# Performance work log

Measured on AMD Instinct MI355X. Metric: run time of the kernel, lower is better.

Reference implementation:

```python
import jax, jax.numpy as jnp
import numpy as np

B, S, E = 2048, 23, 768
RED, H, NUM_LABELS = 256, 8, 25
DH = RED // H
DELTA = 0.1
EPS_LN = 1e-5


def setup_inputs() -> dict:
    key = jax.random.key(0)
    ks = jax.random.split(key, 20)
    g = lambda k, shape, fan: jax.random.normal(k, shape, dtype=jnp.float32) * (1.0 / np.sqrt(fan))
    inp = {
        'cls_embeddings': jax.random.normal(ks[0], (B, S, E), dtype=jnp.float32),
        'existing_mask': jax.random.randint(ks[1], (B, S), 0, 2, dtype=jnp.int32),
        'missing_emb': g(ks[2], (S, E), E),
        'W1': g(ks[3], (E // 2, E), E), 'b1': jnp.zeros((E // 2,), jnp.float32),
        'W2': g(ks[4], (RED, E // 2), E // 2), 'b2': jnp.zeros((RED,), jnp.float32),
        'ln_g': jnp.ones((RED,), jnp.float32), 'ln_b': jnp.zeros((RED,), jnp.float32),
        'Wq': g(ks[5], (RED, RED), RED), 'bq': jnp.zeros((RED,), jnp.float32),
        'Wk': g(ks[6], (RED, RED), RED), 'bk': jnp.zeros((RED,), jnp.float32),
        'Wv': g(ks[7], (RED, RED), RED), 'bv': jnp.zeros((RED,), jnp.float32),
        'Wo': g(ks[8], (RED, RED), RED), 'bo': jnp.zeros((RED,), jnp.float32),
        'Wp': g(ks[9], (NUM_LABELS, RED), RED), 'bp': jnp.zeros((NUM_LABELS,), jnp.float32),
    }
    return inp


def _layer_norm(x, g, b):
    mu = jnp.mean(x, axis=-1, keepdims=True)
    var = jnp.mean(jnp.square(x - mu), axis=-1, keepdims=True)
    return (x - mu) * jax.lax.rsqrt(var + EPS_LN) * g + b


def _forward(cls_embeddings, existing_mask, missing_emb, W1, b1, W2, b2, ln_g, ln_b,
             Wq, bq, Wk, bk, Wv, bv, Wo, bo, Wp, bp):
    exist = existing_mask > 0                              # [B,S] bool
    # Gather: existing sections use BERT CLS, missing slots use learned embeddings
    sec = jnp.where(exist[..., None], cls_embeddings, missing_emb[None])  # [B,S,E]
    # SectionDimReducer (exact-erf GELU as in nn.GELU default)
    h = jax.nn.gelu(sec @ W1.T + b1, approximate=False)
    h = jax.nn.gelu(h @ W2.T + b2, approximate=False)
    red = _layer_norm(h, ln_g, ln_b)                       # [B,S,RED]
    # Tiny MHA: every slot queries the existing sections of its own EHR
    q = (red @ Wq.T + bq).reshape(B, S, H, DH)
    k = (red @ Wk.T + bk).reshape(B, S, H, DH)
    v = (red @ Wv.T + bv).reshape(B, S, H, DH)
    scores = jnp.einsum('bqhd,bkhd->bhqk', q, k) / np.sqrt(DH)
    scores = jnp.where(exist[:, None, None, :], scores, -1e9)
    attn = jax.nn.softmax(scores, axis=-1)                 # [B,H,S,S]
    ctx = jnp.einsum('bhqk,bkhd->bqhd', attn, v).reshape(B, S, RED)
    mha_out = ctx @ Wo.T + bo                              # [B,S,RED]
    # Scatter: only missing slots (of EHRs with >=1 existing section) are replaced
    any_exist = jnp.any(exist, axis=1)                     # [B]
    use_attn = (~exist) & any_exist[:, None]               # [B,S]
    updated = jnp.where(use_attn[..., None], mha_out, red)
    # margin-based orthogonality loss on section embeddings
    norm = updated / jnp.maximum(jnp.linalg.norm(updated, axis=-1, keepdims=True), 1e-8)
    gram = jnp.einsum('bid,bjd->bij', norm, norm)          # [B,S,S]
    off = 1.0 - jnp.eye(S, dtype=updated.dtype)
    loss_orth = jnp.sum(jax.nn.relu(jnp.abs(gram) - DELTA) * off) / (B * S * (S - 1))
    logits = updated.mean(axis=1) @ Wp.T + bp              # [B,NUM_LABELS]
    return loss_orth, logits


def reference(cls_embeddings, existing_mask, missing_emb, W1, b1, W2, b2, ln_g, ln_b,
              Wq, bq, Wk, bk, Wv, bv, Wo, bo, Wp, bp):
    return _forward(cls_embeddings, existing_mask, missing_emb, W1, b1, W2, b2, ln_g, ln_b,
                    Wq, bq, Wk, bk, Wv, bv, Wo, bo, Wp, bp)
```

## Files before the change

kernel.cpp:

```cpp
#include <hip/hip_runtime.h>

typedef unsigned short u16;
typedef unsigned int u32;
typedef __attribute__((ext_vector_type(8))) short short8;
typedef __attribute__((ext_vector_type(4))) float f32x4;

struct __align__(8) us4 { u16 x, y, z, w; };

__device__ __forceinline__ float bf1(u16 v){ return __uint_as_float(((u32)v) << 16); }
__device__ __forceinline__ float bflo(u32 u){ return __uint_as_float(u << 16); }
__device__ __forceinline__ float bfhi(u32 u){ return __uint_as_float(u & 0xFFFF0000u); }
__device__ __forceinline__ u16 fbf(float f){
    u32 u = __float_as_uint(f);
    return (u16)((u + 0x7FFFu + ((u >> 16) & 1u)) >> 16);
}
__device__ __forceinline__ float gelu_exact(float x){
    return 0.5f * x * (1.0f + erff(x * 0.70710678118654752f));
}
__device__ __forceinline__ void unp8(uint4 u, float* f){
    f[0]=bflo(u.x); f[1]=bfhi(u.x); f[2]=bflo(u.y); f[3]=bfhi(u.y);
    f[4]=bflo(u.z); f[5]=bfhi(u.z); f[6]=bflo(u.w); f[7]=bfhi(u.w);
}
__device__ __forceinline__ uint4 pack8(float4 a, float4 b){
    uint4 u;
    u.x = (u32)fbf(a.x) | ((u32)fbf(a.y) << 16);
    u.y = (u32)fbf(a.z) | ((u32)fbf(a.w) << 16);
    u.z = (u32)fbf(b.x) | ((u32)fbf(b.y) << 16);
    u.w = (u32)fbf(b.z) | ((u32)fbf(b.w) << 16);
    return u;
}

#define MFMA16(a, b, c) __builtin_amdgcn_mfma_f32_16x16x32_bf16(a, b, c, 0, 0, 0)
#define QSTR 264
#define CAPROWS 46208


__global__ __launch_bounds__(256) void wconv(
    const float* __restrict__ W1, const float* __restrict__ W2,
    const float* __restrict__ Wq, const float* __restrict__ Wk,
    const float* __restrict__ Wv, const float* __restrict__ Wo,
    const float* __restrict__ Wp, u16* __restrict__ dst,
    const int* __restrict__ mask, int* __restrict__ idx,
    int* __restrict__ rowsrc, int* __restrict__ cnt)
{
    const int i = blockIdx.x * 256 + threadIdx.x;
    if (i < 47104) {
        if (i < 23) rowsrc[i] = -(i + 1);
        if (mask[i] > 0) {
            const int slot = 23 + atomicAdd(cnt, 1);
            idx[i] = slot;
            rowsrc[slot] = i;
        }
    }
    const float* s; int o;
    if      (i < 294912) { s = W1; o = i; }
    else if (i < 393216) { s = W2; o = i - 294912; }
    else if (i < 458752) { s = Wq; o = i - 393216; }
    else if (i < 524288) { s = Wk; o = i - 458752; }
    else if (i < 589824) { s = Wv; o = i - 524288; }
    else if (i < 655360) { s = Wo; o = i - 589824; }
    else                 { s = Wp; o = i - 655360; }
    dst[i] = fbf(s[o]);
}

__global__ __launch_bounds__(256) void gemm1_kernel(
    const float* __restrict__ cls, const int* __restrict__ rowsrc,
    const int* __restrict__ cnt, const float* __restrict__ missing,
    const u16* __restrict__ W, const float* __restrict__ bias,
    u16* __restrict__ C)
{
    const int K = 768, M = 384;
    const int nBase = blockIdx.y * 128;
    if (nBase >= *cnt + 23) return;
    __shared__ u16 As[128 * 40];
    __shared__ u16 Bs[128 * 40];
    const int tid = threadIdx.x;
    const int w = tid >> 6, lane = tid & 63;
    const int mBase = blockIdx.x * 128;
    const int wr = w >> 1, wc = w & 1;
    const int r0 = tid >> 2;
    const int co = (tid & 3) * 8;
    const int frow = lane & 15, quad = lane >> 4;

    const int rs0 = rowsrc[nBase + r0];
    const int rs1 = rowsrc[nBase + r0 + 64];
    const float* ap0 = (rs0 >= 0) ? cls + (size_t)rs0 * 768
                                  : missing + (size_t)(-rs0 - 1) * 768;
    const float* ap1 = (rs1 >= 0) ? cls + (size_t)rs1 * 768
                                  : missing + (size_t)(-rs1 - 1) * 768;
    const u16* bp0 = W + (size_t)(mBase + r0) * K;
    const u16* bp1 = W + (size_t)(mBase + r0 + 64) * K;

    f32x4 acc[4][4];
#pragma unroll
    for (int mt = 0; mt < 4; ++mt)
#pragma unroll
        for (int nt = 0; nt < 4; ++nt) acc[mt][nt] = f32x4{0.f, 0.f, 0.f, 0.f};

    float4 a0a = *(const float4*)(ap0 + co), a0b = *(const float4*)(ap0 + co + 4);
    float4 a1a = *(const float4*)(ap1 + co), a1b = *(const float4*)(ap1 + co + 4);
    uint4 pb0 = *(const uint4*)(bp0 + co), pb1 = *(const uint4*)(bp1 + co);

    for (int k0 = 0; k0 < K; k0 += 32) {
        __syncthreads();
        *(uint4*)(As + r0 * 40 + co) = pack8(a0a, a0b);
        *(uint4*)(As + (r0 + 64) * 40 + co) = pack8(a1a, a1b);
        *(uint4*)(Bs + r0 * 40 + co) = pb0;
        *(uint4*)(Bs + (r0 + 64) * 40 + co) = pb1;
        __syncthreads();
        if (k0 + 32 < K) {
            const int kn = k0 + 32 + co;
            a0a = *(const float4*)(ap0 + kn); a0b = *(const float4*)(ap0 + kn + 4);
            a1a = *(const float4*)(ap1 + kn); a1b = *(const float4*)(ap1 + kn + 4);
            pb0 = *(const uint4*)(bp0 + kn);  pb1 = *(const uint4*)(bp1 + kn);
        }
        short8 af[4], bfv[4];
#pragma unroll
        for (int mt = 0; mt < 4; ++mt)
            af[mt] = *(const short8*)(As + (wr * 64 + mt * 16 + frow) * 40 + quad * 8);
#pragma unroll
        for (int nt = 0; nt < 4; ++nt)
            bfv[nt] = *(const short8*)(Bs + (wc * 64 + nt * 16 + frow) * 40 + quad * 8);
#pragma unroll
        for (int mt = 0; mt < 4; ++mt)
#pragma unroll
            for (int nt = 0; nt < 4; ++nt)
                acc[mt][nt] = MFMA16(af[mt], bfv[nt], acc[mt][nt]);
    }

#pragma unroll
    for (int nt = 0; nt < 4; ++nt) {
        const int col = mBase + wc * 64 + nt * 16 + frow;
        const float bv = bias[col];
#pragma unroll
        for (int mt = 0; mt < 4; ++mt)
#pragma unroll
            for (int reg = 0; reg < 4; ++reg) {
                const int row = nBase + wr * 64 + mt * 16 + quad * 4 + reg;
                C[(size_t)row * M + col] = fbf(gelu_exact(acc[mt][nt][reg] + bv));
            }
    }
}

__global__ __launch_bounds__(256) void gemm_bt(
    const u16* __restrict__ A, const u16* __restrict__ W,
    const float* __restrict__ bias, u16* __restrict__ C, int K, int M,
    const int* __restrict__ cnt)
{
    const int nBase = blockIdx.y * 128;
    if (nBase >= *cnt + 23) return;
    __shared__ u16 As[128 * 40];
    __shared__ u16 Bs[128 * 40];
    const int tid = threadIdx.x;
    const int w = tid >> 6, lane = tid & 63;
    const int mBase = blockIdx.x * 128;
    const int wr = w >> 1, wc = w & 1;
    const int r0 = tid >> 2;
    const int co = (tid & 3) * 8;
    const int frow = lane & 15, quad = lane >> 4;

    f32x4 acc[4][4];
#pragma unroll
    for (int mt = 0; mt < 4; ++mt)
#pragma unroll
        for (int nt = 0; nt < 4; ++nt) acc[mt][nt] = f32x4{0.f, 0.f, 0.f, 0.f};

    uint4 pa0 = *(const uint4*)(A + (size_t)(nBase + r0) * K + co);
    uint4 pa1 = *(const uint4*)(A + (size_t)(nBase + r0 + 64) * K + co);
    uint4 pb0 = *(const uint4*)(W + (size_t)(mBase + r0) * K + co);
    uint4 pb1 = *(const uint4*)(W + (size_t)(mBase + r0 + 64) * K + co);

    for (int k0 = 0; k0 < K; k0 += 32) {
        __syncthreads();
        *(uint4*)(As + r0 * 40 + co) = pa0;
        *(uint4*)(As + (r0 + 64) * 40 + co) = pa1;
        *(uint4*)(Bs + r0 * 40 + co) = pb0;
        *(uint4*)(Bs + (r0 + 64) * 40 + co) = pb1;
        __syncthreads();
        if (k0 + 32 < K) {
            const int kn = k0 + 32 + co;
            pa0 = *(const uint4*)(A + (size_t)(nBase + r0) * K + kn);
            pa1 = *(const uint4*)(A + (size_t)(nBase + r0 + 64) * K + kn);
            pb0 = *(const uint4*)(W + (size_t)(mBase + r0) * K + kn);
            pb1 = *(const uint4*)(W + (size_t)(mBase + r0 + 64) * K + kn);
        }
        short8 af[4], bfv[4];
#pragma unroll
        for (int mt = 0; mt < 4; ++mt)
            af[mt] = *(const short8*)(As + (wr * 64 + mt * 16 + frow) * 40 + quad * 8);
#pragma unroll
        for (int nt = 0; nt < 4; ++nt)
            bfv[nt] = *(const short8*)(Bs + (wc * 64 + nt * 16 + frow) * 40 + quad * 8);
#pragma unroll
        for (int mt = 0; mt < 4; ++mt)
#pragma unroll
            for (int nt = 0; nt < 4; ++nt)
                acc[mt][nt] = MFMA16(af[mt], bfv[nt], acc[mt][nt]);
    }

#pragma unroll
    for (int nt = 0; nt < 4; ++nt) {
        const int col = mBase + wc * 64 + nt * 16 + frow;
        const float bv = bias[col];
#pragma unroll
        for (int mt = 0; mt < 4; ++mt)
#pragma unroll
            for (int reg = 0; reg < 4; ++reg) {
                const int row = nBase + wr * 64 + mt * 16 + quad * 4 + reg;
                C[(size_t)row * M + col] = fbf(gelu_exact(acc[mt][nt][reg] + bv));
            }
    }
}

__device__ __forceinline__ void ln1_reg(
    const float* x, const float4& g0, const float4& g1,
    const float4& b0, const float4& b1, u16* rp)
{
    float s = x[0] + x[1] + x[2] + x[3] + x[4] + x[5] + x[6] + x[7];
    s += __shfl_xor(s, 1); s += __shfl_xor(s, 2); s += __shfl_xor(s, 4);
    s += __shfl_xor(s, 8); s += __shfl_xor(s, 16);
    const float mu = s * (1.f / 256.f);
    float v = 0.f;
#pragma unroll
    for (int e = 0; e < 8; ++e) { const float d = x[e] - mu; v += d * d; }
    v += __shfl_xor(v, 1); v += __shfl_xor(v, 2); v += __shfl_xor(v, 4);
    v += __shfl_xor(v, 8); v += __shfl_xor(v, 16);
    const float rs = rsqrtf(v * (1.f / 256.f) + 1e-5f);
    float4 ya, yb;
    ya.x = (x[0]-mu)*rs*g0.x + b0.x;
    ya.y = (x[1]-mu)*rs*g0.y + b0.y;
    ya.z = (x[2]-mu)*rs*g0.z + b0.z;
    ya.w = (x[3]-mu)*rs*g0.w + b0.w;
    yb.x = (x[4]-mu)*rs*g1.x + b1.x;
    yb.y = (x[5]-mu)*rs*g1.y + b1.y;
    yb.z = (x[6]-mu)*rs*g1.z + b1.z;
    yb.w = (x[7]-mu)*rs*g1.w + b1.w;
    *(uint4*)rp = pack8(ya, yb);
}

__device__ __forceinline__ void ln3_reg_store(
    uint4 rg0, uint4 rg1, uint4 rg2, bool has2,
    const float* __restrict__ lng, const float* __restrict__ lnb,
    u16* dstBase, int s0, int c0o)
{
    const float4 g0 = *(const float4*)(lng + c0o);
    const float4 g1 = *(const float4*)(lng + c0o + 4);
    const float4 b0 = *(const float4*)(lnb + c0o);
    const float4 b1 = *(const float4*)(lnb + c0o + 4);
    float x[8];
    unp8(rg0, x); ln1_reg(x, g0, g1, b0, b1, dstBase + s0 * QSTR + c0o);
    unp8(rg1, x); ln1_reg(x, g0, g1, b0, b1, dstBase + (s0 + 8) * QSTR + c0o);
    if (has2) { unp8(rg2, x); ln1_reg(x, g0, g1, b0, b1, dstBase + (s0 + 16) * QSTR + c0o); }
}

#define KLOOP_PF(WPTR, SRC, ACC)                                                  \
    {                                                                             \
        short8 nb0 = *(const short8*)(WPTR);                                      \
        short8 nb1 = *(const short8*)((WPTR) + 16 * 256);                         \
        short8 nb2 = *(const short8*)((WPTR) + 32 * 256);                         \
        short8 nb3 = *(const short8*)((WPTR) + 48 * 256);                         \
        for (int k0 = 0; k0 < 256; k0 += 32) {                                    \
            short8 a0 = *(const short8*)((SRC) + r0c * QSTR + k0 + quad * 8);     \
            short8 a1 = *(const short8*)((SRC) + r1c * QSTR + k0 + quad * 8);     \
            short8 c0 = nb0, c1 = nb1, c2 = nb2, c3 = nb3;                        \
            if (k0 + 32 < 256) {                                                  \
                nb0 = *(const short8*)((WPTR) + (k0 + 32));                       \
                nb1 = *(const short8*)((WPTR) + 16 * 256 + (k0 + 32));            \
                nb2 = *(const short8*)((WPTR) + 32 * 256 + (k0 + 32));            \
                nb3 = *(const short8*)((WPTR) + 48 * 256 + (k0 + 32));            \
            }                                                                     \
            ACC[0][0] = MFMA16(a0, c0, ACC[0][0]); ACC[1][0] = MFMA16(a1, c0, ACC[1][0]); \
            ACC[0][1] = MFMA16(a0, c1, ACC[0][1]); ACC[1][1] = MFMA16(a1, c1, ACC[1][1]); \
            ACC[0][2] = MFMA16(a0, c2, ACC[0][2]); ACC[1][2] = MFMA16(a1, c2, ACC[1][2]); \
            ACC[0][3] = MFMA16(a0, c3, ACC[0][3]); ACC[1][3] = MFMA16(a1, c3, ACC[1][3]); \
        }                                                                         \
    }

__global__ __launch_bounds__(256, 3) void attn_tail_kernel(
    const u16* __restrict__ redb, const int* __restrict__ mask,
    const int* __restrict__ idxArr,
    const u16* __restrict__ Wqkvb,
    const float* __restrict__ bq, const float* __restrict__ bk,
    const float* __restrict__ bv, const u16* __restrict__ Wob,
    const float* __restrict__ bo, const float* __restrict__ lng,
    const float* __restrict__ lnb, const u16* __restrict__ Wpb,
    const float* __restrict__ bp, float* __restrict__ out,
    float* __restrict__ lossAcc)
{
    __shared__ __align__(16) unsigned char SM[40960];
    u16* s_rq = (u16*)SM;
    u16* s_k  = (u16*)(SM + 12144);
    u16* s_vT = (u16*)(SM + 24288);
    int* sEx   = (int*)(SM + 40672);
    int* sMiss = (int*)(SM + 40764);
    int* sCrow = (int*)(SM + 40856);
    float* sDiag = (float*)(SM + 24288);
    float* sInv  = (float*)(SM + 24384);
    float* sPool = (float*)(SM + 24480);

    const int b = blockIdx.x, t = threadIdx.x;
    const int w = t >> 6, lane = t & 63;
    const int frow = lane & 15, quad = lane >> 4;
    const int r0c = frow;
    const int r1c = (16 + frow > 22) ? 22 : 16 + frow;
    const f32x4 z4 = f32x4{0.f, 0.f, 0.f, 0.f};

    {
        const int myEx = (t < 23) ? mask[b * 23 + t] : 0;
        if (t < 23) {
            sEx[t] = myEx;
            sCrow[t] = (myEx > 0) ? idxArr[b * 23 + t] : t;
        }
        if (t < 64) {
            const unsigned long long ball = __ballot((t < 23) && (myEx > 0));
            if (t < 23) sMiss[t] = (ball != 0ull && myEx <= 0) ? 1 : 0;
        }
    }
    for (int i = t; i < 1024; i += 256) ((uint4*)s_vT)[i] = make_uint4(0u, 0u, 0u, 0u);
    __syncthreads();

    {
        const int s0 = t >> 5, c0o = (t & 31) * 8;
        uint4 rg0 = *(const uint4*)(redb + (size_t)sCrow[s0] * 256 + c0o);
        uint4 rg1 = *(const uint4*)(redb + (size_t)sCrow[s0 + 8] * 256 + c0o);
        uint4 rg2 = make_uint4(0u, 0u, 0u, 0u);
        const bool has2 = t < 224;
        if (has2) rg2 = *(const uint4*)(redb + (size_t)sCrow[s0 + 16] * 256 + c0o);
        ln3_reg_store(rg0, rg1, rg2, has2, lng, lnb, s_rq, s0, c0o);
    }
    __syncthreads();

    const int cmb = w * 64 + frow;
    {
        f32x4 ka[2][4];
#pragma unroll
        for (int mt = 0; mt < 2; ++mt)
#pragma unroll
            for (int nt = 0; nt < 4; ++nt) ka[mt][nt] = z4;
        const u16* wp = Wqkvb + (size_t)(256 + cmb) * 256 + quad * 8;
        const float bb[4] = {bk[cmb], bk[cmb + 16], bk[cmb + 32], bk[cmb + 48]};
        KLOOP_PF(wp, s_rq, ka)
#pragma unroll
        for (int nt = 0; nt < 4; ++nt) {
            const int cm = cmb + nt * 16;
#pragma unroll
            for (int mt = 0; mt < 2; ++mt)
#pragma unroll
                for (int reg = 0; reg < 4; ++reg) {
                    const int s = mt * 16 + quad * 4 + reg;
                    if (s < 23) s_k[s * QSTR + cm] = fbf(ka[mt][nt][reg] + bb[nt]);
                }
        }
    }
    {
        f32x4 va[2][4];
#pragma unroll
        for (int mt = 0; mt < 2; ++mt)
#pragma unroll
            for (int nt = 0; nt < 4; ++nt) va[mt][nt] = z4;
        const u16* wp = Wqkvb + (size_t)(512 + cmb) * 256 + quad * 8;
        const float bb[4] = {bv[cmb], bv[cmb + 16], bv[cmb + 32], bv[cmb + 48]};
        KLOOP_PF(wp, s_rq, va)
#pragma unroll
        for (int nt = 0; nt < 4; ++nt) {
            const int cm = cmb + nt * 16;
#pragma unroll
            for (int mt = 0; mt < 2; ++mt)
#pragma unroll
                for (int reg = 0; reg < 4; ++reg) {
                    const int s = mt * 16 + quad * 4 + reg;
                    if (s < 23) s_vT[cm * 32 + s] = fbf(va[mt][nt][reg] + bb[nt]);
                }
        }
    }
    {
        f32x4 qa[2][4];
#pragma unroll
        for (int mt = 0; mt < 2; ++mt)
#pragma unroll
            for (int nt = 0; nt < 4; ++nt) qa[mt][nt] = z4;
        const u16* wp = Wqkvb + (size_t)cmb * 256 + quad * 8;
        const float bb[4] = {bq[cmb], bq[cmb + 16], bq[cmb + 32], bq[cmb + 48]};
        KLOOP_PF(wp, s_rq, qa)
        __syncthreads();
#pragma unroll
        for (int nt = 0; nt < 4; ++nt) {
            const int cm = cmb + nt * 16;
#pragma unroll
            for (int mt = 0; mt < 2; ++mt)
#pragma unroll
                for (int reg = 0; reg < 4; ++reg) {
                    const int s = mt * 16 + quad * 4 + reg;
                    if (s < 23) s_rq[s * QSTR + cm] = fbf(qa[mt][nt][reg] + bb[nt]);
                }
        }
    }

    {
        const float scl = 0.17677669529663687f;
        const float m0 = (sEx[frow] > 0) ? 0.f : -1e9f;
        const float m1 = (16 + frow < 23 && sEx[16 + frow] > 0) ? 0.f : -1e9f;
#pragma unroll
        for (int hh2 = 0; hh2 < 2; ++hh2) {
            const int hb = w * 64 + hh2 * 32;
            short8 aq0 = *(const short8*)(s_rq + r0c * QSTR + hb + quad * 8);
            short8 aq1 = *(const short8*)(s_rq + r1c * QSTR + hb + quad * 8);
            short8 bk0 = *(const short8*)(s_k + r0c * QSTR + hb + quad * 8);
            short8 bk1 = *(const short8*)(s_k + r1c * QSTR + hb + quad * 8);
            f32x4 s00 = MFMA16(aq0, bk0, z4);
            f32x4 s01 = MFMA16(aq0, bk1, z4);
            f32x4 s10 = MFMA16(aq1, bk0, z4);
            f32x4 s11 = MFMA16(aq1, bk1, z4);
#pragma unroll
            for (int mt = 0; mt < 2; ++mt) {
                f32x4& c0 = mt ? s10 : s00;
                f32x4& c1 = mt ? s11 : s01;
#pragma unroll
                for (int reg = 0; reg < 4; ++reg) {
                    float v0 = c0[reg] * scl + m0;
                    float v1 = c1[reg] * scl + m1;
                    float mx = fmaxf(v0, v1);
#pragma unroll
                    for (int m = 8; m; m >>= 1) mx = fmaxf(mx, __shfl_xor(mx, m));
                    float p0 = __expf(v0 - mx), p1 = __expf(v1 - mx);
                    float sm = p0 + p1;
#pragma unroll
                    for (int m = 8; m; m >>= 1) sm += __shfl_xor(sm, m);
                    const float inv = 1.f / sm;
                    c0[reg] = p0 * inv;
                    c1[reg] = p1 * inv;
                }
            }
#pragma unroll
            for (int reg = 0; reg < 4; ++reg) {
                const int q0r = quad * 4 + reg;
                s_k[q0r * QSTR + hb + frow]      = fbf(s00[reg]);
                s_k[q0r * QSTR + hb + 16 + frow] = fbf(s01[reg]);
                const int q1r = 16 + quad * 4 + reg;
                if (q1r < 23) {
                    s_k[q1r * QSTR + hb + frow]      = fbf(s10[reg]);
                    s_k[q1r * QSTR + hb + 16 + frow] = fbf(s11[reg]);
                }
            }
            short8 pa0 = *(const short8*)(s_k + r0c * QSTR + hb + quad * 8);
            short8 pa1 = *(const short8*)(s_k + r1c * QSTR + hb + quad * 8);
            short8 bv0 = *(const short8*)(s_vT + (hb + frow) * 32 + quad * 8);
            short8 bv1 = *(const short8*)(s_vT + (hb + 16 + frow) * 32 + quad * 8);
            f32x4 c00 = MFMA16(pa0, bv0, z4);
            f32x4 c01 = MFMA16(pa0, bv1, z4);
            f32x4 c10 = MFMA16(pa1, bv0, z4);
            f32x4 c11 = MFMA16(pa1, bv1, z4);
#pragma unroll
            for (int reg = 0; reg < 4; ++reg) {
                const int q0r = quad * 4 + reg;
                s_rq[q0r * QSTR + hb + frow]      = fbf(c00[reg]);
                s_rq[q0r * QSTR + hb + 16 + frow] = fbf(c01[reg]);
                const int q1r = 16 + quad * 4 + reg;
                if (q1r < 23) {
                    s_rq[q1r * QSTR + hb + frow]      = fbf(c10[reg]);
                    s_rq[q1r * QSTR + hb + 16 + frow] = fbf(c11[reg]);
                }
            }
        }
    }
    __syncthreads();

    {
        f32x4 wacc[2][4];
#pragma unroll
        for (int mt = 0; mt < 2; ++mt)
#pragma unroll
            for (int nt = 0; nt < 4; ++nt) wacc[mt][nt] = z4;
        const u16* wp = Wob + (size_t)cmb * 256 + quad * 8;
        const float ob[4] = {bo[cmb], bo[cmb + 16], bo[cmb + 32], bo[cmb + 48]};
        KLOOP_PF(wp, s_rq, wacc)
        {
            const int s0 = t >> 5, c0o = (t & 31) * 8;
            uint4 rg0 = *(const uint4*)(redb + (size_t)sCrow[s0] * 256 + c0o);
            uint4 rg1 = *(const uint4*)(redb + (size_t)sCrow[s0 + 8] * 256 + c0o);
            uint4 rg2 = make_uint4(0u, 0u, 0u, 0u);
            const bool has2 = t < 224;
            if (has2) rg2 = *(const uint4*)(redb + (size_t)sCrow[s0 + 16] * 256 + c0o);
            ln3_reg_store(rg0, rg1, rg2, has2, lng, lnb, s_k, s0, c0o);
        }
        __syncthreads();
#pragma unroll
        for (int nt = 0; nt < 4; ++nt) {
            const int col = cmb + nt * 16;
#pragma unroll
            for (int mt = 0; mt < 2; ++mt)
#pragma unroll
                for (int reg = 0; reg < 4; ++reg) {
                    const int s = mt * 16 + quad * 4 + reg;
                    if (s < 23 && sMiss[s])
                        s_k[s * QSTR + col] = fbf(wacc[mt][nt][reg] + ob[nt]);
                }
        }
    }
    __syncthreads();

    f32x4 g00 = z4, g01 = z4, g10 = z4, g11 = z4;
    if (w == 0) {
        short8 ga0 = *(const short8*)(s_k + r0c * QSTR + quad * 8);
        short8 ga1 = *(const short8*)(s_k + r1c * QSTR + quad * 8);
        for (int k0 = 0; k0 < 256; k0 += 32) {
            short8 a0 = ga0, a1 = ga1;
            if (k0 + 32 < 256) {
                ga0 = *(const short8*)(s_k + r0c * QSTR + k0 + 32 + quad * 8);
                ga1 = *(const short8*)(s_k + r1c * QSTR + k0 + 32 + quad * 8);
            }
            g00 = MFMA16(a0, a0, g00);
            g01 = MFMA16(a0, a1, g01);
            g10 = MFMA16(a1, a0, g10);
            g11 = MFMA16(a1, a1, g11);
        }
#pragma unroll
        for (int reg = 0; reg < 4; ++reg) {
            if (frow == quad * 4 + reg) {
                sDiag[frow] = g00[reg];
                if (16 + frow < 23) sDiag[16 + frow] = g11[reg];
            }
        }
    } else {
        for (int c = t - 64; c < 256; c += 192) {
            float pv = 0.f;
#pragma unroll
            for (int s = 0; s < 23; ++s) pv += bf1(s_k[s * QSTR + c]);
            sPool[c] = pv * (1.f / 23.f);
        }
    }
    __syncthreads();
    if (t < 23) sInv[t] = 1.f / fmaxf(sqrtf(sDiag[t]), 1e-8f);
    __syncthreads();

    if (w == 0) {
        float contrib = 0.f;
        const float ic0 = sInv[frow];
        const float ic1 = (16 + frow < 23) ? sInv[16 + frow] : 0.f;
        const bool c1ok = (16 + frow < 23);
#pragma unroll
        for (int reg = 0; reg < 4; ++reg) {
            const int rA = quad * 4 + reg;
            const float irA = sInv[rA];
            if (rA != frow) {
                const float cc = fabsf(g00[reg] * irA * ic0) - 0.1f;
                if (cc > 0.f) contrib += cc;
            }
            if (c1ok) {
                const float cc = fabsf(g01[reg] * irA * ic1) - 0.1f;
                if (cc > 0.f) contrib += cc;
            }
            const int rB = 16 + quad * 4 + reg;
            if (rB < 23) {
                const float irB = sInv[rB];
                {
                    const float cc = fabsf(g10[reg] * irB * ic0) - 0.1f;
                    if (cc > 0.f) contrib += cc;
                }
                if (c1ok && rB != 16 + frow) {
                    const float cc = fabsf(g11[reg] * irB * ic1) - 0.1f;
                    if (cc > 0.f) contrib += cc;
                }
            }
        }
#pragma unroll
        for (int m = 32; m; m >>= 1) contrib += __shfl_xor(contrib, m);
        if (lane == 0) atomicAdd(lossAcc, contrib);
    } else {
        const int li = t - 64;
        {
            const int L = li >> 3, chunk = li & 7;
            float a = 0.f;
#pragma unroll
            for (int q4 = 0; q4 < 4; ++q4) {
                const int c8 = chunk * 4 + q4;
                float wf[8]; unp8(*(const uint4*)(Wpb + (size_t)L * 256 + c8 * 8), wf);
                const float4 p0 = *(const float4*)(sPool + c8 * 8);
                const float4 p1 = *(const float4*)(sPool + c8 * 8 + 4);
                a += wf[0] * p0.x + wf[1] * p0.y + wf[2] * p0.z + wf[3] * p0.w
                   + wf[4] * p1.x + wf[5] * p1.y + wf[6] * p1.z + wf[7] * p1.w;
            }
            a += __shfl_xor(a, 1); a += __shfl_xor(a, 2); a += __shfl_xor(a, 4);
            if (chunk == 0) out[1 + b * 25 + L] = a + bp[L];
        }
        if (li < 8) {
            float a = 0.f;
#pragma unroll
            for (int q4 = 0; q4 < 4; ++q4) {
                const int c8 = li * 4 + q4;
                float wf[8]; unp8(*(const uint4*)(Wpb + (size_t)24 * 256 + c8 * 8), wf);
                const float4 p0 = *(const float4*)(sPool + c8 * 8);
                const float4 p1 = *(const float4*)(sPool + c8 * 8 + 4);
                a += wf[0] * p0.x + wf[1] * p0.y + wf[2] * p0.z + wf[3] * p0.w
                   + wf[4] * p1.x + wf[5] * p1.y + wf[6] * p1.z + wf[7] * p1.w;
            }
            a += __shfl_xor(a, 1); a += __shfl_xor(a, 2); a += __shfl_xor(a, 4);
            if (li == 0) out[1 + b * 25 + 24] = a + bp[24];
        }
    }
}

__global__ void loss_finalize(const float* __restrict__ lossAcc, float* __restrict__ out)
{
    out[0] = lossAcc[0] * (1.f / 1036288.f);
}

extern "C" void kernel_launch(void* const* d_in, const int* in_sizes, int n_in,
                              void* d_out, int out_size, void* d_ws, size_t ws_size,
                              hipStream_t stream)
{
    const float* cls     = (const float*)d_in[0];
    const int*   mask    = (const int*)d_in[1];
    const float* missing = (const float*)d_in[2];
    const float* W1 = (const float*)d_in[3];  const float* b1 = (const float*)d_in[4];
    const float* W2 = (const float*)d_in[5];  const float* b2 = (const float*)d_in[6];
    const float* lng = (const float*)d_in[7]; const float* lnb = (const float*)d_in[8];
    const float* Wq = (const float*)d_in[9];  const float* bq = (const float*)d_in[10];
    const float* Wk = (const float*)d_in[11]; const float* bk = (const float*)d_in[12];
    const float* Wv = (const float*)d_in[13]; const float* bv = (const float*)d_in[14];
    const float* Wo = (const float*)d_in[15]; const float* bo = (const float*)d_in[16];
    const float* Wp = (const float*)d_in[17]; const float* bp = (const float*)d_in[18];
    float* out = (float*)d_out;

    char* ws = (char*)d_ws;
    u16* h1b  = (u16*)ws;
    u16* redb = (u16*)(ws + 35487744);
    u16* Wb   = (u16*)(ws + 59146240);
    u16* W1b   = Wb;
    u16* W2b   = Wb + 294912;
    u16* Wqkvb = Wb + 393216;
    u16* Wob   = Wb + 589824;
    u16* Wpb   = Wb + 655360;
    int* idx    = (int*)(ws + 60469760);
    int* rowsrc = (int*)(ws + 60658176);
    int* cnt    = (int*)(ws + 60843008);
    float* lossAcc = (float*)(ws + 60843012);

    hipMemsetAsync(cnt, 0, 8, stream);
    hipMemsetAsync(rowsrc, 0, CAPROWS * sizeof(int), stream);

    wconv<<<2585, 256, 0, stream>>>(W1, W2, Wq, Wk, Wv, Wo, Wp, Wb,
                                    mask, idx, rowsrc, cnt);
    gemm1_kernel<<<dim3(3, 361), 256, 0, stream>>>(cls, rowsrc, cnt, missing,
                                                   W1b, b1, h1b);
    gemm_bt<<<dim3(2, 361), 256, 0, stream>>>(h1b, W2b, b2, redb, 384, 256, cnt);
    attn_tail_kernel<<<2048, 256, 0, stream>>>(redb, mask, idx, Wqkvb, bq, bk, bv,
                                               Wob, bo, lng, lnb, Wpb, bp,
                                               out, lossAcc);
    loss_finalize<<<1, 1, 0, stream>>>(lossAcc, out);
}
```

Baseline: 501.4 us.

## Double-buffer A tiles and load W fragments directly into registers in GEMMs

Both GEMM kernels now double-buffer the A tile in shared memory, so each k-step needs one barrier instead of two. The B (weight) operand no longer goes through shared memory: each lane loads its MFMA fragment straight from global memory into registers and prefetches the next step's fragment. This removes LDS traffic and a sync per iteration. In exchange it issues more global loads of the weight matrix, since the two warp rows duplicate them, and raises register pressure.

```diff
diff --git a/kernel.cpp b/kernel.cpp
--- a/kernel.cpp
+++ b/kernel.cpp
@@ -72,8 +72,7 @@
     const int K = 768, M = 384;
     const int nBase = blockIdx.y * 128;
     if (nBase >= *cnt + 23) return;
-    __shared__ u16 As[128 * 40];
-    __shared__ u16 Bs[128 * 40];
+    __shared__ u16 As[2][128 * 40];
     const int tid = threadIdx.x;
     const int w = tid >> 6, lane = tid & 63;
     const int mBase = blockIdx.x * 128;
@@ -88,8 +87,7 @@
                                   : missing + (size_t)(-rs0 - 1) * 768;
     const float* ap1 = (rs1 >= 0) ? cls + (size_t)rs1 * 768
                                   : missing + (size_t)(-rs1 - 1) * 768;
-    const u16* bp0 = W + (size_t)(mBase + r0) * K;
-    const u16* bp1 = W + (size_t)(mBase + r0 + 64) * K;
+    const u16* wpB = W + (size_t)(mBase + wc * 64 + frow) * K + quad * 8;
 
     f32x4 acc[4][4];
 #pragma unroll
@@ -97,35 +95,50 @@
 #pragma unroll
         for (int nt = 0; nt < 4; ++nt) acc[mt][nt] = f32x4{0.f, 0.f, 0.f, 0.f};
 
-    float4 a0a = *(const float4*)(ap0 + co), a0b = *(const float4*)(ap0 + co + 4);
-    float4 a1a = *(const float4*)(ap1 + co), a1b = *(const float4*)(ap1 + co + 4);
-    uint4 pb0 = *(const uint4*)(bp0 + co), pb1 = *(const uint4*)(bp1 + co);
+    {
+        float4 p0a = *(const float4*)(ap0 + co), p0b = *(const float4*)(ap0 + co + 4);
+        float4 p1a = *(const float4*)(ap1 + co), p1b = *(const float4*)(ap1 + co + 4);
+        *(uint4*)(As[0] + r0 * 40 + co) = pack8(p0a, p0b);
+        *(uint4*)(As[0] + (r0 + 64) * 40 + co) = pack8(p1a, p1b);
+    }
+    short8 nb0 = *(const short8*)(wpB);
+    short8 nb1 = *(const short8*)(wpB + 16 * K);
+    short8 nb2 = *(const short8*)(wpB + 32 * K);
+    short8 nb3 = *(const short8*)(wpB + 48 * K);
+    __syncthreads();
 
     for (int k0 = 0; k0 < K; k0 += 32) {
-        __syncthreads();
-        *(uint4*)(As + r0 * 40 + co) = pack8(a0a, a0b);
-        *(uint4*)(As + (r0 + 64) * 40 + co) = pack8(a1a, a1b);
-        *(uint4*)(Bs + r0 * 40 + co) = pb0;
-        *(uint4*)(Bs + (r0 + 64) * 40 + co) = pb1;
-        __syncthreads();
-        if (k0 + 32 < K) {
+        const int cur = (k0 >> 5) & 1;
+        const bool more = (k0 + 32) < K;
+        float4 a0a = make_float4(0.f,0.f,0.f,0.f), a0b = a0a, a1a = a0a, a1b = a0a;
+        if (more) {
             const int kn = k0 + 32 + co;
             a0a = *(const float4*)(ap0 + kn); a0b = *(const float4*)(ap0 + kn + 4);
             a1a = *(const float4*)(ap1 + kn); a1b = *(const float4*)(ap1 + kn + 4);
-            pb0 = *(const uint4*)(bp0 + kn);  pb1 = *(const uint4*)(bp1 + kn);
-        }
-        short8 af[4], bfv[4];
+        }
+        short8 c0 = nb0, c1 = nb1, c2 = nb2, c3 = nb3;
+        if (more) {
+            nb0 = *(const short8*)(wpB + (k0 + 32));
+            nb1 = *(const short8*)(wpB + 16 * K + (k0 + 32));
+            nb2 = *(const short8*)(wpB + 32 * K + (k0 + 32));
+            nb3 = *(const short8*)(wpB + 48 * K + (k0 + 32));
+        }
+        short8 af[4];
 #pragma unroll
         for (int mt = 0; mt < 4; ++mt)
-            af[mt] = *(const short8*)(As + (wr * 64 + mt * 16 + frow) * 40 + quad * 8);
-#pragma unroll
-        for (int nt = 0; nt < 4; ++nt)
-            bfv[nt] = *(const short8*)(Bs + (wc * 64 + nt * 16 + frow) * 40 + quad * 8);
-#pragma unroll
-        for (int mt = 0; mt < 4; ++mt)
-#pragma unroll
-            for (int nt = 0; nt < 4; ++nt)
-                acc[mt][nt] = MFMA16(af[mt], bfv[nt], acc[mt][nt]);
+            af[mt] = *(const short8*)(As[cur] + (wr * 64 + mt * 16 + frow) * 40 + quad * 8);
+#pragma unroll
+        for (int mt = 0; mt < 4; ++mt) {
+            acc[mt][0] = MFMA16(af[mt], c0, acc[mt][0]);
+            acc[mt][1] = MFMA16(af[mt], c1, acc[mt][1]);
+            acc[mt][2] = MFMA16(af[mt], c2, acc[mt][2]);
+            acc[mt][3] = MFMA16(af[mt], c3, acc[mt][3]);
+        }
+        if (more) {
+            *(uint4*)(As[cur ^ 1] + r0 * 40 + co) = pack8(a0a, a0b);
+            *(uint4*)(As[cur ^ 1] + (r0 + 64) * 40 + co) = pack8(a1a, a1b);
+            __syncthreads();
+        }
     }
 
 #pragma unroll
@@ -149,8 +162,7 @@
 {
     const int nBase = blockIdx.y * 128;
     if (nBase >= *cnt + 23) return;
-    __shared__ u16 As[128 * 40];
-    __shared__ u16 Bs[128 * 40];
+    __shared__ u16 As[2][128 * 40];
     const int tid = threadIdx.x;
     const int w = tid >> 6, lane = tid & 63;
     const int mBase = blockIdx.x * 128;
@@ -159,43 +171,56 @@
     const int co = (tid & 3) * 8;
     const int frow = lane & 15, quad = lane >> 4;
 
+    const u16* apA0 = A + (size_t)(nBase + r0) * K;
+    const u16* apA1 = A + (size_t)(nBase + r0 + 64) * K;
+    const u16* wpB = W + (size_t)(mBase + wc * 64 + frow) * K + quad * 8;
+
     f32x4 acc[4][4];
 #pragma unroll
     for (int mt = 0; mt < 4; ++mt)
 #pragma unroll
         for (int nt = 0; nt < 4; ++nt) acc[mt][nt] = f32x4{0.f, 0.f, 0.f, 0.f};
 
-    uint4 pa0 = *(const uint4*)(A + (size_t)(nBase + r0) * K + co);
-    uint4 pa1 = *(const uint4*)(A + (size_t)(nBase + r0 + 64) * K + co);
-    uint4 pb0 = *(const uint4*)(W + (size_t)(mBase + r0) * K + co);
-    uint4 pb1 = *(const uint4*)(W + (size_t)(mBase + r0 + 64) * K + co);
+    *(uint4*)(As[0] + r0 * 40 + co) = *(const uint4*)(apA0 + co);
+    *(uint4*)(As[0] + (r0 + 64) * 40 + co) = *(const uint4*)(apA1 + co);
+    short8 nb0 = *(const short8*)(wpB);
+    short8 nb1 = *(const short8*)(wpB + 16 * K);
+    short8 nb2 = *(const short8*)(wpB + 32 * K);
+    short8 nb3 = *(const short8*)(wpB + 48 * K);
+    __syncthreads();
 
     for (int k0 = 0; k0 < K; k0 += 32) {
-        __syncthreads();
-        *(uint4*)(As + r0 * 40 + co) = pa0;
-        *(uint4*)(As + (r0 + 64) * 40 + co) = pa1;
-        *(uint4*)(Bs + r0 * 40 + co) = pb0;
-        *(uint4*)(Bs + (r0 + 64) * 40 + co) = pb1;
-        __syncthreads();
-        if (k0 + 32 < K) {
+        const int cur = (k0 >> 5) & 1;
+        const bool more = (k0 + 32) < K;
+        uint4 ua0 = make_uint4(0u,0u,0u,0u), ua1 = ua0;
+        if (more) {
             const int kn = k0 + 32 + co;
-            pa0 = *(const uint4*)(A + (size_t)(nBase + r0) * K + kn);
-            pa1 = *(const uint4*)(A + (size_t)(nBase + r0 + 64) * K + kn);
-            pb0 = *(const uint4*)(W + (size_t)(mBase + r0) * K + kn);
-            pb1 = *(const uint4*)(W + (size_t)(mBase + r0 + 64) * K + kn);
-        }
-        short8 af[4], bfv[4];
+            ua0 = *(const uint4*)(apA0 + kn);
+            ua1 = *(const uint4*)(apA1 + kn);
+        }
+        short8 c0 = nb0, c1 = nb1, c2 = nb2, c3 = nb3;
+        if (more) {
+            nb0 = *(const short8*)(wpB + (k0 + 32));
+            nb1 = *(const short8*)(wpB + 16 * K + (k0 + 32));
+            nb2 = *(const short8*)(wpB + 32 * K + (k0 + 32));
+            nb3 = *(const short8*)(wpB + 48 * K + (k0 + 32));
+        }
+        short8 af[4];
 #pragma unroll
         for (int mt = 0; mt < 4; ++mt)
-            af[mt] = *(const short8*)(As + (wr * 64 + mt * 16 + frow) * 40 + quad * 8);
-#pragma unroll
-        for (int nt = 0; nt < 4; ++nt)
-            bfv[nt] = *(const short8*)(Bs + (wc * 64 + nt * 16 + frow) * 40 + quad * 8);
-#pragma unroll
-        for (int mt = 0; mt < 4; ++mt)
-#pragma unroll
-            for (int nt = 0; nt < 4; ++nt)
-                acc[mt][nt] = MFMA16(af[mt], bfv[nt], acc[mt][nt]);
+            af[mt] = *(const short8*)(As[cur] + (wr * 64 + mt * 16 + frow) * 40 + quad * 8);
+#pragma unroll
+        for (int mt = 0; mt < 4; ++mt) {
+            acc[mt][0] = MFMA16(af[mt], c0, acc[mt][0]);
+            acc[mt][1] = MFMA16(af[mt], c1, acc[mt][1]);
+            acc[mt][2] = MFMA16(af[mt], c2, acc[mt][2]);
+            acc[mt][3] = MFMA16(af[mt], c3, acc[mt][3]);
+        }
+        if (more) {
+            *(uint4*)(As[cur ^ 1] + r0 * 40 + co) = ua0;
+            *(uint4*)(As[cur ^ 1] + (r0 + 64) * 40 + co) = ua1;
+            __syncthreads();
+        }
     }
 
 #pragma unroll
```

Result: slower. 630.9 us (+25.8%).
